# Optimization experiments

Measured on AMD Instinct MI355X. Metric: run time of the kernel, lower is better.

Reference implementation:

```python
import jax, jax.numpy as jnp
import numpy as np

NUM_GROUPS = 8
EPS = 1e-5
QB = 128.0  # 2 ** (8 - 1), b = 8 activation bits


def setup_inputs() -> dict:
    key = jax.random.key(0)
    k1, k2, k3 = jax.random.split(key, 3)
    B, IN, OUT = 8192, 4096, 4096
    x = jax.random.normal(k1, (B, IN), jnp.float32)
    # emulates the int8 sign buffer (values in {-1, +1}) stored as float
    qw = jnp.sign(jax.random.normal(k2, (OUT, IN), jnp.float32))
    bias = jax.random.normal(k3, (OUT,), jnp.float32) * 0.02
    return {"x": x, "qw": qw, "bias": bias}


def _ste_sign(z):
    # straight-through estimator: sign in fwd, identity grad in bwd
    return jax.lax.stop_gradient(jnp.sign(z) - z) + z


def reference(x, qw, bias):
    g = NUM_GROUPS
    # dequantize_weights: global mean-abs scale over the sign buffer
    alpha = jnp.mean(jnp.abs(qw))
    w = qw * alpha                                  # [OUT, IN]
    OUT, IN = w.shape
    # binarize_weights_groupwise: groups along out_features rows
    wg = w.reshape(g, OUT // g, IN)
    alpha_g = jnp.mean(jnp.abs(wg), axis=(1, 2), keepdims=True)
    bw = _ste_sign(wg - alpha_g).reshape(OUT, IN)   # values in {-1, 0, +1}
    # linear
    out = x @ bw.T + bias                           # [B, OUT]
    # quantize_activations_groupwise: groups along batch dim, b=8
    B = out.shape[0]
    og = out.reshape(g, B // g, OUT)
    gamma_g = jnp.max(jnp.abs(og), axis=(1, 2), keepdims=True)
    q = jnp.clip(og * QB / (gamma_g + EPS), -QB + EPS, QB - EPS)
    return q.reshape(B, OUT)
```

## Files before the change

### kernel.cpp

```cpp
#include <hip/hip_runtime.h>
#include <hip/hip_bf16.h>
#include <stdint.h>

#define B_DIM   8192
#define IN_DIM  4096
#define OUT_DIM 4096
#define QB_V    128.0f
#define EPS_V   1e-5f

typedef __attribute__((ext_vector_type(4))) float  f32x4;
typedef __attribute__((ext_vector_type(8))) __bf16 bf16x8;

__device__ __forceinline__ void gload_lds16(const void* g, void* l) {
  void* gp = const_cast<void*>(g);
  __builtin_amdgcn_global_load_lds(
      (__attribute__((address_space(1))) void*)gp,
      (__attribute__((address_space(3))) void*)l, 16, 0, 0);
}

__device__ __forceinline__ __bf16 sgnb(float d) {
  return (__bf16)((d > 0.f) ? 1.f : (d < 0.f ? -1.f : 0.f));
}

__global__ void k_init(unsigned* ws) {
  int t = threadIdx.x;
  if (t < 16) ws[t] = 0u;
}

__global__ __launch_bounds__(256) void k_qw_sums(const float* __restrict__ qw,
                                                 float* __restrict__ sums) {
  __shared__ float red[4];
  const int t = threadIdx.x;
  for (int vb = blockIdx.x; vb < 4096; vb += 2048) {
    const size_t base = (size_t)vb * 4096;
    float s = 0.f;
#pragma unroll
    for (int j = 0; j < 4; ++j) {
      f32x4 v = *(const f32x4*)(qw + base + (size_t)j * 1024 + t * 4);
      s += fabsf(v.x) + fabsf(v.y) + fabsf(v.z) + fabsf(v.w);
    }
#pragma unroll
    for (int off = 32; off > 0; off >>= 1) s += __shfl_xor(s, off);
    __syncthreads();
    if ((t & 63) == 0) red[t >> 6] = s;
    __syncthreads();
    if (t == 0)
      atomicAdd(sums + (vb >> 9), red[0] + red[1] + red[2] + red[3]);
  }
}

__global__ __launch_bounds__(256) void k_conv(const float* __restrict__ qw,
                                              const float* __restrict__ sums,
                                              __bf16* __restrict__ bw,
                                              const float* __restrict__ x,
                                              __bf16* __restrict__ xb) {
  const int t = threadIdx.x;
  for (int vb = blockIdx.x; vb < 12288; vb += 2048) {
    if (vb < 4096) {
      const size_t i = ((size_t)vb * 256 + t) * 16;
      const float mu = sums[(int)(i >> 21)] * (1.0f / 2097152.0f);
#pragma unroll
      for (int h = 0; h < 2; ++h) {
        f32x4 v0 = *(const f32x4*)(qw + i + h * 8);
        f32x4 v1 = *(const f32x4*)(qw + i + h * 8 + 4);
        bf16x8 r;
        r[0] = sgnb(v0.x - mu); r[1] = sgnb(v0.y - mu);
        r[2] = sgnb(v0.z - mu); r[3] = sgnb(v0.w - mu);
        r[4] = sgnb(v1.x - mu); r[5] = sgnb(v1.y - mu);
        r[6] = sgnb(v1.z - mu); r[7] = sgnb(v1.w - mu);
        *(bf16x8*)(bw + i + h * 8) = r;
      }
    } else {
      const size_t i = ((size_t)(vb - 4096) * 256 + t) * 16;
#pragma unroll
      for (int h = 0; h < 2; ++h) {
        f32x4 v0 = *(const f32x4*)(x + i + h * 8);
        f32x4 v1 = *(const f32x4*)(x + i + h * 8 + 4);
        bf16x8 r;
        r[0] = (__bf16)v0.x; r[1] = (__bf16)v0.y;
        r[2] = (__bf16)v0.z; r[3] = (__bf16)v0.w;
        r[4] = (__bf16)v1.x; r[5] = (__bf16)v1.y;
        r[6] = (__bf16)v1.z; r[7] = (__bf16)v1.w;
        *(bf16x8*)(xb + i + h * 8) = r;
      }
    }
  }
}

__global__ __launch_bounds__(512, 2) void k_gemm256(
    const __bf16* __restrict__ xa, const __bf16* __restrict__ bwb,
    const float* __restrict__ bias, float* __restrict__ out,
    unsigned* __restrict__ gamma_bits) {
  __shared__ __bf16 As[2][256 * 64];
  __shared__ __bf16 Bs[2][256 * 64];
  const int t = threadIdx.x;
  const int lane = t & 63;
  const int wv = t >> 6;
  const int wr = wv >> 2;
  const int wc = wv & 3;
  const int fr = lane & 15, fq = lane >> 4;
  const int fr7 = fr & 7;

  const int orig = blockIdx.x;
  const int bid = ((orig & 7) << 6) | (orig >> 3);
  const int bm = bid & 31, bn = bid >> 5;
  const int brow = bm << 8, bcol = bn << 8;

  const int srow = t >> 3;
  const int cchunk = t & 7;
  const int schunk = cchunk ^ (srow & 7);
  const int dstoff = (srow << 6) + (cchunk << 3);
  const __bf16* aRow = xa + (size_t)(brow + srow) * IN_DIM + (schunk << 3);
  const __bf16* bRow = bwb + (size_t)(bcol + srow) * IN_DIM + (schunk << 3);

#define STAGE_A(kt, dd)                                                     \
  {                                                                         \
    const int _k0 = (kt) << 6;                                              \
    _Pragma("unroll") for (int r = 0; r < 4; ++r)                           \
        gload_lds16(aRow + (size_t)(r << 6) * IN_DIM + _k0,                 \
                    &As[dd][(r << 12) + dstoff]);                           \
  }
#define STAGE_B(kt, dd)                                                     \
  {                                                                         \
    const int _k0 = (kt) << 6;                                              \
    _Pragma("unroll") for (int r = 0; r < 4; ++r)                           \
        gload_lds16(bRow + (size_t)(r << 6) * IN_DIM + _k0,                 \
                    &Bs[dd][(r << 12) + dstoff]);                           \
  }

  f32x4 acc[8][4] = {};

  STAGE_A(0, 0);
  STAGE_B(0, 0);

  int d = 0;
  for (int kt = 0; kt < 64; ++kt) {
    __builtin_amdgcn_s_barrier();
    if (kt < 63) {
      STAGE_A(kt + 1, d ^ 1);
      asm volatile("s_waitcnt vmcnt(4)" ::: "memory");
    } else {
      asm volatile("s_waitcnt vmcnt(0)" ::: "memory");
    }
    __builtin_amdgcn_s_barrier();

#pragma unroll
    for (int ks = 0; ks < 2; ++ks) {
      const int cs = (ks << 2) | fq;
      bf16x8 af[8], bfv[4];
#pragma unroll
      for (int m = 0; m < 8; ++m)
        af[m] = *(const bf16x8*)(&As[d][(((wr << 7) + (m << 4) + fr) << 6) +
                                        ((cs ^ fr7) << 3)]);
#pragma unroll
      for (int n = 0; n < 4; ++n)
        bfv[n] = *(const bf16x8*)(&Bs[d][(((wc << 6) + (n << 4) + fr) << 6) +
                                         ((cs ^ fr7) << 3)]);
      __builtin_amdgcn_s_setprio(1);
#pragma unroll
      for (int m = 0; m < 8; ++m)
#pragma unroll
        for (int n = 0; n < 4; ++n)
          acc[m][n] = __builtin_amdgcn_mfma_f32_16x16x32_bf16(
              af[m], bfv[n], acc[m][n], 0, 0, 0);
      __builtin_amdgcn_s_setprio(0);
      if (ks == 0 && kt < 63) STAGE_B(kt + 1, d ^ 1);
    }
    d ^= 1;
  }
#undef STAGE_A
#undef STAGE_B

  float mx = 0.f;
  const int colbase = bcol + (wc << 6);
#pragma unroll
  for (int n = 0; n < 4; ++n) {
    const int col = colbase + (n << 4) + fr;
    const float bv = bias[col];
#pragma unroll
    for (int m = 0; m < 8; ++m) {
      const int rowb = brow + (wr << 7) + (m << 4) + (fq << 2);
#pragma unroll
      for (int j = 0; j < 4; ++j) {
        const float v = acc[m][n][j] + bv;
        out[(size_t)(rowb + j) * OUT_DIM + col] = v;
        mx = fmaxf(mx, fabsf(v));
      }
    }
  }
#pragma unroll
  for (int off = 32; off > 0; off >>= 1) mx = fmaxf(mx, __shfl_xor(mx, off));
  if (lane == 0)
    atomicMax(gamma_bits + (brow >> 10), __float_as_uint(mx));
}

__global__ __launch_bounds__(256) void k_scale(float* __restrict__ out,
                                               const unsigned* __restrict__ gb) {
  const int t = threadIdx.x;
  for (int vb = blockIdx.x; vb < 8192; vb += 2048) {
    const size_t i = ((size_t)vb * 256 + t) * 16;
    const float gamma = __uint_as_float(gb[(int)(i >> 22)]);
    const float sc = QB_V / (gamma + EPS_V);
    const float lo = -QB_V + EPS_V, hi = QB_V - EPS_V;
#pragma unroll
    for (int h = 0; h < 4; ++h) {
      f32x4 v = *(const f32x4*)(out + i + h * 4);
      v.x = fminf(fmaxf(v.x * sc, lo), hi);
      v.y = fminf(fmaxf(v.y * sc, lo), hi);
      v.z = fminf(fmaxf(v.z * sc, lo), hi);
      v.w = fminf(fmaxf(v.w * sc, lo), hi);
      *(f32x4*)(out + i + h * 4) = v;
    }
  }
}

extern "C" void kernel_launch(void* const* d_in, const int* in_sizes, int n_in,
                              void* d_out, int out_size, void* d_ws,
                              size_t ws_size, hipStream_t stream) {
  const float* x = (const float*)d_in[0];
  const float* qw = (const float*)d_in[1];
  const float* bias = (const float*)d_in[2];
  float* out = (float*)d_out;
  char* ws = (char*)d_ws;
  float* sums = (float*)ws;
  unsigned* gamma = (unsigned*)ws + 8;
  __bf16* bwb = (__bf16*)(ws + 256);
  __bf16* xb = (__bf16*)(ws + 256 + (size_t)OUT_DIM * IN_DIM * 2);

  k_init<<<1, 64, 0, stream>>>((unsigned*)ws);
  k_qw_sums<<<2048, 256, 0, stream>>>(qw, sums);
  k_conv<<<2048, 256, 0, stream>>>(qw, sums, bwb, x, xb);
  k_gemm256<<<512, 512, 0, stream>>>(xb, bwb, bias, out, gamma);
  k_scale<<<2048, 256, 0, stream>>>(out, gamma);
}
```

Baseline: 701.2 us.

## Use 4-stage K=32 LDS pipeline with split B fragment loads in GEMM

Restructures the bf16 GEMM mainloop from a double-buffered K=64 tile into a four-slot ring of K=32 tiles, prefetching three tiles ahead, with a new XOR swizzle for the 32-wide rows. Each tile's MFMA work is split into two halves, and A/B staging and B fragment reads are interleaved with barriers between them. The aim is to hide global-to-LDS latency and overlap loads with matrix math. The cost is more barriers per K step, plus a risk of bank conflicts or hazards from the new swizzle and staging order.

```diff
diff --git a/kernel.cpp b/kernel.cpp
--- a/kernel.cpp
+++ b/kernel.cpp
@@ -91,85 +91,103 @@
     const __bf16* __restrict__ xa, const __bf16* __restrict__ bwb,
     const float* __restrict__ bias, float* __restrict__ out,
     unsigned* __restrict__ gamma_bits) {
-  __shared__ __bf16 As[2][256 * 64];
-  __shared__ __bf16 Bs[2][256 * 64];
+  __shared__ __bf16 As[4][256 * 32];
+  __shared__ __bf16 Bs[4][256 * 32];
   const int t = threadIdx.x;
   const int lane = t & 63;
   const int wv = t >> 6;
   const int wr = wv >> 2;
   const int wc = wv & 3;
   const int fr = lane & 15, fq = lane >> 4;
-  const int fr7 = fr & 7;
+  const int swz8 = (fq ^ ((fr >> 1) & 3)) << 3;
 
   const int orig = blockIdx.x;
   const int bid = ((orig & 7) << 6) | (orig >> 3);
   const int bm = bid & 31, bn = bid >> 5;
   const int brow = bm << 8, bcol = bn << 8;
 
-  const int srow = t >> 3;
-  const int cchunk = t & 7;
-  const int schunk = cchunk ^ (srow & 7);
-  const int dstoff = (srow << 6) + (cchunk << 3);
-  const __bf16* aRow = xa + (size_t)(brow + srow) * IN_DIM + (schunk << 3);
-  const __bf16* bRow = bwb + (size_t)(bcol + srow) * IN_DIM + (schunk << 3);
-
-#define STAGE_A(kt, dd)                                                     \
-  {                                                                         \
-    const int _k0 = (kt) << 6;                                              \
-    _Pragma("unroll") for (int r = 0; r < 4; ++r)                           \
-        gload_lds16(aRow + (size_t)(r << 6) * IN_DIM + _k0,                 \
-                    &As[dd][(r << 12) + dstoff]);                           \
-  }
-#define STAGE_B(kt, dd)                                                     \
-  {                                                                         \
-    const int _k0 = (kt) << 6;                                              \
-    _Pragma("unroll") for (int r = 0; r < 4; ++r)                           \
-        gload_lds16(bRow + (size_t)(r << 6) * IN_DIM + _k0,                 \
-                    &Bs[dd][(r << 12) + dstoff]);                           \
+  const int srow = t >> 2;
+  const int schunk8 = ((t & 3) ^ ((t >> 3) & 3)) << 3;
+  const int doff0 = t * 8;
+  const int doff1 = doff0 + 128 * 32;
+  const __bf16* aR0 = xa + (size_t)(brow + srow) * IN_DIM + schunk8;
+  const __bf16* aR1 = aR0 + (size_t)128 * IN_DIM;
+  const __bf16* bR0 = bwb + (size_t)(bcol + srow) * IN_DIM + schunk8;
+  const __bf16* bR1 = bR0 + (size_t)128 * IN_DIM;
+
+#define STAGE_A(kt, sl)                          \
+  {                                              \
+    const int _k = (kt) << 5;                    \
+    gload_lds16(aR0 + _k, &As[sl][doff0]);       \
+    gload_lds16(aR1 + _k, &As[sl][doff1]);       \
+  }
+#define STAGE_B(kt, sl)                          \
+  {                                              \
+    const int _k = (kt) << 5;                    \
+    gload_lds16(bR0 + _k, &Bs[sl][doff0]);       \
+    gload_lds16(bR1 + _k, &Bs[sl][doff1]);       \
   }
 
   f32x4 acc[8][4] = {};
 
-  STAGE_A(0, 0);
-  STAGE_B(0, 0);
-
-  int d = 0;
-  for (int kt = 0; kt < 64; ++kt) {
-    __builtin_amdgcn_s_barrier();
-    if (kt < 63) {
-      STAGE_A(kt + 1, d ^ 1);
-      asm volatile("s_waitcnt vmcnt(4)" ::: "memory");
-    } else {
-      asm volatile("s_waitcnt vmcnt(0)" ::: "memory");
-    }
-    __builtin_amdgcn_s_barrier();
-
-#pragma unroll
-    for (int ks = 0; ks < 2; ++ks) {
-      const int cs = (ks << 2) | fq;
-      bf16x8 af[8], bfv[4];
-#pragma unroll
-      for (int m = 0; m < 8; ++m)
-        af[m] = *(const bf16x8*)(&As[d][(((wr << 7) + (m << 4) + fr) << 6) +
-                                        ((cs ^ fr7) << 3)]);
-#pragma unroll
-      for (int n = 0; n < 4; ++n)
-        bfv[n] = *(const bf16x8*)(&Bs[d][(((wc << 6) + (n << 4) + fr) << 6) +
-                                         ((cs ^ fr7) << 3)]);
-      __builtin_amdgcn_s_setprio(1);
-#pragma unroll
-      for (int m = 0; m < 8; ++m)
-#pragma unroll
-        for (int n = 0; n < 4; ++n)
-          acc[m][n] = __builtin_amdgcn_mfma_f32_16x16x32_bf16(
-              af[m], bfv[n], acc[m][n], 0, 0, 0);
-      __builtin_amdgcn_s_setprio(0);
-      if (ks == 0 && kt < 63) STAGE_B(kt + 1, d ^ 1);
-    }
-    d ^= 1;
-  }
+#define TILE_BODY(kt, sl, DOSTAGE)                                            \
+  {                                                                           \
+    bf16x8 af[8], bf01[2], bf23[2];                                           \
+    if (DOSTAGE) STAGE_A((kt) + 3, ((kt) + 3) & 3);                           \
+    _Pragma("unroll") for (int m = 0; m < 8; ++m)                             \
+        af[m] = *(const bf16x8*)(&As[sl][((wr << 7) + (m << 4) + fr) * 32 +   \
+                                         swz8]);                              \
+    _Pragma("unroll") for (int n = 0; n < 2; ++n)                             \
+        bf01[n] = *(const bf16x8*)(&Bs[sl][((wc << 6) + (n << 4) + fr) * 32 + \
+                                           swz8]);                            \
+    __builtin_amdgcn_s_barrier();                                             \
+    __builtin_amdgcn_s_setprio(1);                                            \
+    _Pragma("unroll") for (int m = 0; m < 8; ++m)                             \
+      _Pragma("unroll") for (int n = 0; n < 2; ++n)                           \
+          acc[m][n] = __builtin_amdgcn_mfma_f32_16x16x32_bf16(                \
+              af[m], bf01[n], acc[m][n], 0, 0, 0);                            \
+    __builtin_amdgcn_s_setprio(0);                                            \
+    __builtin_amdgcn_s_barrier();                                             \
+    if (DOSTAGE) STAGE_B((kt) + 3, ((kt) + 3) & 3);                           \
+    _Pragma("unroll") for (int n = 0; n < 2; ++n)                             \
+        bf23[n] = *(const bf16x8*)(&Bs[sl][((wc << 6) + ((n + 2) << 4) + fr) *\
+                                               32 + swz8]);                   \
+    __builtin_amdgcn_s_barrier();                                             \
+    __builtin_amdgcn_s_setprio(1);                                            \
+    _Pragma("unroll") for (int m = 0; m < 8; ++m)                             \
+      _Pragma("unroll") for (int n = 0; n < 2; ++n)                           \
+          acc[m][n + 2] = __builtin_amdgcn_mfma_f32_16x16x32_bf16(            \
+              af[m], bf23[n], acc[m][n + 2], 0, 0, 0);                        \
+    __builtin_amdgcn_s_setprio(0);                                            \
+  }
+#define BOUNDARY(N)                                        \
+  asm volatile("s_waitcnt vmcnt(" #N ")" ::: "memory");    \
+  __builtin_amdgcn_s_barrier();
+
+  STAGE_A(0, 0); STAGE_B(0, 0);
+  STAGE_A(1, 1); STAGE_B(1, 1);
+  STAGE_A(2, 2); STAGE_B(2, 2);
+  BOUNDARY(8)
+
+  for (int ktb = 0; ktb < 124; ktb += 4) {
+#pragma unroll
+    for (int u = 0; u < 4; ++u) {
+      TILE_BODY(ktb + u, u, true)
+      BOUNDARY(8)
+    }
+  }
+  TILE_BODY(124, 0, true)
+  BOUNDARY(8)
+  TILE_BODY(125, 1, false)
+  BOUNDARY(4)
+  TILE_BODY(126, 2, false)
+  BOUNDARY(0)
+  TILE_BODY(127, 3, false)
+
 #undef STAGE_A
 #undef STAGE_B
+#undef TILE_BODY
+#undef BOUNDARY
 
   float mx = 0.f;
   const int colbase = bcol + (wc << 6);
```

Result: slower. 720.8 us (+2.8%).
